# Optimization experiments

Hardware: AMD Instinct MI355X
Metric: run time of the kernel (lower is better)

The kernel has to match this reference:

```python
import jax, jax.numpy as jnp
import numpy as np

D_MODEL = 4096
NUM_EXPERTS = 64
TOP_K = 2


def setup_inputs() -> dict:
    key = jax.random.key(0)
    kx, kw, kb = jax.random.split(key, 3)
    x = jax.random.normal(kx, (4, 4096, D_MODEL), dtype=jnp.float32)
    # nn.Linear default init ~ U(-1/sqrt(fan_in), 1/sqrt(fan_in))
    bound = 1.0 / np.sqrt(D_MODEL)
    W = jax.random.uniform(kw, (D_MODEL, NUM_EXPERTS), minval=-bound, maxval=bound, dtype=jnp.float32)
    b = jax.random.uniform(kb, (NUM_EXPERTS,), minval=-bound, maxval=bound, dtype=jnp.float32)
    return {"x": x, "W": W, "b": b}


def reference(x, W, b):
    # gate: [B,S,D] @ [D,E] -> [B,S,E]
    logits = jnp.einsum('bsd,de->bse', x, W) + b
    probs = jax.nn.softmax(logits, axis=-1)
    topk_probs, topk_indices = jax.lax.top_k(probs, TOP_K)
    topk_probs = topk_probs / (jnp.sum(topk_probs, axis=-1, keepdims=True) + 1e-9)
    return probs, topk_probs, topk_indices
```

## Files before the change

### kernel.cpp

```cpp
#include <hip/hip_runtime.h>

#define D_MODEL 4096
#define NEXP    64
#define NTOK    16384
#define NKS     128

typedef _Float16 half8 __attribute__((ext_vector_type(8)));
typedef float    f32x4 __attribute__((ext_vector_type(4)));

__device__ __forceinline__ void split8(float4 a, float4 b, half8& hi, half8& lo) {
    auto h0 = __builtin_amdgcn_cvt_pkrtz(a.x, a.y);
    auto h1 = __builtin_amdgcn_cvt_pkrtz(a.z, a.w);
    auto h2 = __builtin_amdgcn_cvt_pkrtz(b.x, b.y);
    auto h3 = __builtin_amdgcn_cvt_pkrtz(b.z, b.w);
    hi[0] = static_cast<_Float16>(h0[0]); hi[1] = static_cast<_Float16>(h0[1]);
    hi[2] = static_cast<_Float16>(h1[0]); hi[3] = static_cast<_Float16>(h1[1]);
    hi[4] = static_cast<_Float16>(h2[0]); hi[5] = static_cast<_Float16>(h2[1]);
    hi[6] = static_cast<_Float16>(h3[0]); hi[7] = static_cast<_Float16>(h3[1]);
    float r0 = a.x - (float)h0[0], r1 = a.y - (float)h0[1];
    float r2 = a.z - (float)h1[0], r3 = a.w - (float)h1[1];
    float r4 = b.x - (float)h2[0], r5 = b.y - (float)h2[1];
    float r6 = b.z - (float)h3[0], r7 = b.w - (float)h3[1];
    auto l0 = __builtin_amdgcn_cvt_pkrtz(r0, r1);
    auto l1 = __builtin_amdgcn_cvt_pkrtz(r2, r3);
    auto l2 = __builtin_amdgcn_cvt_pkrtz(r4, r5);
    auto l3 = __builtin_amdgcn_cvt_pkrtz(r6, r7);
    lo[0] = static_cast<_Float16>(l0[0]); lo[1] = static_cast<_Float16>(l0[1]);
    lo[2] = static_cast<_Float16>(l1[0]); lo[3] = static_cast<_Float16>(l1[1]);
    lo[4] = static_cast<_Float16>(l2[0]); lo[5] = static_cast<_Float16>(l2[1]);
    lo[6] = static_cast<_Float16>(l3[0]); lo[7] = static_cast<_Float16>(l3[1]);
}

__device__ __forceinline__ void dma16(const float* g, float* l) {
    __builtin_amdgcn_global_load_lds(
        (const __attribute__((address_space(1))) unsigned int*)g,
        (__attribute__((address_space(3))) unsigned int*)l,
        16, 0, 0);
}

__global__ __launch_bounds__(256) void prep_w(const float* __restrict__ W,
                                              half8* __restrict__ ws) {
    const int gid  = blockIdx.x * 256 + threadIdx.x;
    const int lane = gid & 63;
    const int fp   = gid >> 6;
    const int t    = fp & 3;
    const int ks   = fp >> 2;
    const int e    = 16 * t + (lane & 15);
    const int k0   = ks * 32 + (lane >> 4) * 8;
    float4 a, b;
    a.x = W[(size_t)(k0 + 0) * NEXP + e];
    a.y = W[(size_t)(k0 + 1) * NEXP + e];
    a.z = W[(size_t)(k0 + 2) * NEXP + e];
    a.w = W[(size_t)(k0 + 3) * NEXP + e];
    b.x = W[(size_t)(k0 + 4) * NEXP + e];
    b.y = W[(size_t)(k0 + 5) * NEXP + e];
    b.z = W[(size_t)(k0 + 6) * NEXP + e];
    b.w = W[(size_t)(k0 + 7) * NEXP + e];
    half8 hi, lo;
    split8(a, b, hi, lo);
    ws[(size_t)(fp * 2 + 0) * 64 + lane] = hi;
    ws[(size_t)(fp * 2 + 1) * 64 + lane] = lo;
}

__global__ __launch_bounds__(256, 2) void router_mfma(
    const float* __restrict__ x, const int4* __restrict__ wf,
    const float* __restrict__ b, float* __restrict__ out)
{
    __shared__ float lds[4][4096];
    const int tid  = threadIdx.x;
    const int lane = tid & 63;
    const int wv   = tid >> 6;
    const int tok0 = blockIdx.x * 16;
    const int m    = lane & 15;
    const int q    = lane >> 4;
    const float* __restrict__ xrow =
        x + (size_t)(tok0 + m) * D_MODEL + wv * 1024 + q * 8;
    const int4* __restrict__ wq = wf + (size_t)wv * 32 * 512 + lane;
    float* __restrict__ xs = lds[wv];

    const int rot = (blockIdx.x ^ wv) & 7;

    f32x4 acc[4] = {};
    int4  wba[4][2], wbb[4][2];

    auto jof = [&](int bb) { return ((bb + rot) & 7) * 4; };

    auto stage = [&](int bb, int buf) {
        const int j0 = jof(bb);
        float* dst = xs + buf * 2048;
#pragma unroll
        for (int s = 0; s < 4; s++) {
            const float* src = xrow + (size_t)(j0 + s) * 32;
            dma16(src,     dst + (s * 2 + 0) * 256);
            dma16(src + 4, dst + (s * 2 + 1) * 256);
        }
    };
    auto ldw = [&](int4 (&w)[4][2], int j) {
        const int base = j * 512;
#pragma unroll
        for (int t = 0; t < 4; t++) {
            w[t][0] = wq[base + t * 128];
            w[t][1] = wq[base + t * 128 + 64];
        }
    };
    auto cmp = [&](int buf, int slot, int4 (&wb)[4][2]) {
        const float* px = xs + buf * 2048 + slot * 512 + lane * 4;
        float4 xa = *(const float4*)px;
        float4 xb = *(const float4*)(px + 256);
        half8 ahi, alo;
        split8(xa, xb, ahi, alo);
#pragma unroll
        for (int t = 0; t < 4; t++) {
            half8 bhi = __builtin_bit_cast(half8, wb[t][0]);
            half8 blo = __builtin_bit_cast(half8, wb[t][1]);
            acc[t] = __builtin_amdgcn_mfma_f32_16x16x32_f16(ahi, bhi, acc[t], 0, 0, 0);
            acc[t] = __builtin_amdgcn_mfma_f32_16x16x32_f16(ahi, blo, acc[t], 0, 0, 0);
            acc[t] = __builtin_amdgcn_mfma_f32_16x16x32_f16(alo, bhi, acc[t], 0, 0, 0);
        }
    };

    stage(0, 0);
    ldw(wba, jof(0));

#pragma unroll 1
    for (int bb = 0; bb < 8; bb++) {
        const int buf = bb & 1;
        if (bb < 7) {
            stage(bb + 1, buf ^ 1);
            asm volatile("s_waitcnt vmcnt(8)" ::: "memory");
        } else {
            asm volatile("s_waitcnt vmcnt(0)" ::: "memory");
        }
        __builtin_amdgcn_sched_barrier(0);
        const int j0 = jof(bb);
        const int jn = jof((bb + 1) & 7);
        ldw(wbb, j0 + 1); cmp(buf, 0, wba);
        ldw(wba, j0 + 2); cmp(buf, 1, wbb);
        ldw(wbb, j0 + 3); cmp(buf, 2, wba);
        ldw(wba, jn);     cmp(buf, 3, wbb);
    }

#pragma unroll
    for (int t = 0; t < 4; t++)
#pragma unroll
        for (int r = 0; r < 4; r++)
            xs[(q * 4 + r) * 68 + t * 16 + m] = acc[t][r];
    __syncthreads();

    const float bias = b[lane];
    float* __restrict__ probs_out = out;
    float* __restrict__ top_out   = out + (size_t)NTOK * NEXP;
    float* __restrict__ idx_out   = top_out + (size_t)NTOK * 2;

#pragma unroll 1
    for (int r2 = 0; r2 < 4; r2++) {
        const int row   = wv * 4 + r2;
        const int token = tok0 + row;
        float logit = lds[0][row * 68 + lane] + lds[1][row * 68 + lane]
                    + lds[2][row * 68 + lane] + lds[3][row * 68 + lane] + bias;

        float mx = logit;
#pragma unroll
        for (int off = 32; off; off >>= 1) mx = fmaxf(mx, __shfl_xor(mx, off, 64));
        float ex = expf(logit - mx);
        float s = ex;
#pragma unroll
        for (int off = 32; off; off >>= 1) s += __shfl_xor(s, off, 64);
        float p = ex / s;
        probs_out[(size_t)token * NEXP + lane] = p;

        float v = p; int idx = lane;
#pragma unroll
        for (int off = 32; off; off >>= 1) {
            float ov = __shfl_xor(v, off, 64);
            int   oi = __shfl_xor(idx, off, 64);
            if (ov > v || (ov == v && oi < idx)) { v = ov; idx = oi; }
        }
        const float v1 = v; const int i1 = idx;
        v = (lane == i1) ? -1.0f : p; idx = lane;
#pragma unroll
        for (int off = 32; off; off >>= 1) {
            float ov = __shfl_xor(v, off, 64);
            int   oi = __shfl_xor(idx, off, 64);
            if (ov > v || (ov == v && oi < idx)) { v = ov; idx = oi; }
        }
        const float v2 = v; const int i2 = idx;

        if (lane == 0) {
            const float dnm = v1 + v2 + 1e-9f;
            top_out[(size_t)token * 2 + 0] = v1 / dnm;
            top_out[(size_t)token * 2 + 1] = v2 / dnm;
            idx_out[(size_t)token * 2 + 0] = (float)i1;
            idx_out[(size_t)token * 2 + 1] = (float)i2;
        }
    }
}

#define BK  128
#define BKP (BK + 4)
__device__ __forceinline__ float rl(float v, int l) {
    return __int_as_float(__builtin_amdgcn_readlane(__float_as_int(v), l));
}
__global__ __launch_bounds__(128) void router_fallback(
    const float* __restrict__ x, const float* __restrict__ W,
    const float* __restrict__ b, float* __restrict__ out)
{
    __shared__ float wt[NEXP * BKP];
    const int tid  = threadIdx.x;
    const int lane = tid & 63;
    const int wv   = __builtin_amdgcn_readfirstlane(tid >> 6);
    const int tok0 = blockIdx.x * 16 + wv * 8;
    const float* __restrict__ xw = x + (size_t)tok0 * D_MODEL;

    float2 xcur[8], xnxt[8];
#pragma unroll
    for (int t = 0; t < 8; t++)
        xcur[t] = *(const float2*)(xw + (size_t)t * D_MODEL + 2 * lane);
    float accm[8];
#pragma unroll
    for (int t = 0; t < 8; t++) accm[t] = 0.f;

    for (int c = 0; c < D_MODEL / BK; c++) {
        const int k0 = c * BK;
        if (c + 1 < D_MODEL / BK) {
#pragma unroll
            for (int t = 0; t < 8; t++)
                xnxt[t] = *(const float2*)(xw + (size_t)t * D_MODEL + (k0 + BK) + 2 * lane);
        }
#pragma unroll
        for (int i = 0; i < 16; i++) {
            int n  = i * 128 + tid;
            int dd = n >> 4;
            int e0 = (n & 15) * 4;
            float4 v = *(const float4*)(W + (size_t)(k0 + dd) * NEXP + e0);
            wt[(e0 + 0) * BKP + dd] = v.x;
            wt[(e0 + 1) * BKP + dd] = v.y;
            wt[(e0 + 2) * BKP + dd] = v.z;
            wt[(e0 + 3) * BKP + dd] = v.w;
        }
        __syncthreads();
        float acc[8];
#pragma unroll
        for (int t = 0; t < 8; t++) acc[t] = 0.f;
        const float* wl = &wt[lane * BKP];
#pragma unroll 4
        for (int kk = 0; kk < BK; kk += 4) {
            float4 w4 = *(const float4*)(wl + kk);
            const int l0 = kk >> 1;
#pragma unroll
            for (int t = 0; t < 8; t++) {
                float a = acc[t];
                a = fmaf(rl(xcur[t].x, l0    ), w4.x, a);
                a = fmaf(rl(xcur[t].y, l0    ), w4.y, a);
                a = fmaf(rl(xcur[t].x, l0 + 1), w4.z, a);
                a = fmaf(rl(xcur[t].y, l0 + 1), w4.w, a);
                acc[t] = a;
            }
        }
#pragma unroll
        for (int t = 0; t < 8; t++) accm[t] += acc[t];
        __syncthreads();
#pragma unroll
        for (int t = 0; t < 8; t++) xcur[t] = xnxt[t];
    }

    const float bias = b[lane];
    float* __restrict__ probs_out = out;
    float* __restrict__ top_out   = out + (size_t)NTOK * NEXP;
    float* __restrict__ idx_out   = top_out + (size_t)NTOK * 2;
#pragma unroll 1
    for (int t = 0; t < 8; t++) {
        const int token = tok0 + t;
        float logit = accm[t] + bias;
        float mx = logit;
#pragma unroll
        for (int off = 32; off; off >>= 1) mx = fmaxf(mx, __shfl_xor(mx, off, 64));
        float ex = expf(logit - mx);
        float s = ex;
#pragma unroll
        for (int off = 32; off; off >>= 1) s += __shfl_xor(s, off, 64);
        float p = ex / s;
        probs_out[(size_t)token * NEXP + lane] = p;
        float v = p; int idx = lane;
#pragma unroll
        for (int off = 32; off; off >>= 1) {
            float ov = __shfl_xor(v, off, 64);
            int   oi = __shfl_xor(idx, off, 64);
            if (ov > v || (ov == v && oi < idx)) { v = ov; idx = oi; }
        }
        const float v1 = v; const int i1 = idx;
        v = (lane == i1) ? -1.0f : p; idx = lane;
#pragma unroll
        for (int off = 32; off; off >>= 1) {
            float ov = __shfl_xor(v, off, 64);
            int   oi = __shfl_xor(idx, off, 64);
            if (ov > v || (ov == v && oi < idx)) { v = ov; idx = oi; }
        }
        const float v2 = v; const int i2 = idx;
        if (lane == 0) {
            const float dnm = v1 + v2 + 1e-9f;
            top_out[(size_t)token * 2 + 0] = v1 / dnm;
            top_out[(size_t)token * 2 + 1] = v2 / dnm;
            idx_out[(size_t)token * 2 + 0] = (float)i1;
            idx_out[(size_t)token * 2 + 1] = (float)i2;
        }
    }
}

extern "C" void kernel_launch(void* const* d_in, const int* in_sizes, int n_in,
                              void* d_out, int out_size, void* d_ws, size_t ws_size,
                              hipStream_t stream) {
    const float* x = (const float*)d_in[0];
    const float* W = (const float*)d_in[1];
    const float* b = (const float*)d_in[2];
    float* out = (float*)d_out;

    const size_t need = (size_t)NKS * 4 * 2 * 64 * 16;
    if (ws_size >= need) {
        prep_w<<<128, 256, 0, stream>>>(W, (half8*)d_ws);
        router_mfma<<<NTOK / 16, 256, 0, stream>>>(x, (const int4*)d_ws, b, out);
    } else {
        router_fallback<<<NTOK / 16, 128, 0, stream>>>(x, W, b, out);
    }
}
```

Measured before the change: 392.0 us.

## Process 32 tokens per block to reuse loaded W fragments across two token tiles

Each block now handles 32 tokens instead of 16, with two accumulator sets, so every W fragment loaded into registers feeds two MFMA token tiles. This halves the W fetch traffic per token and the grid size. The x staging layout, rotation, and loop trip counts are restructured so each stage covers two k-chunks for both token tiles. In exchange it uses more accumulator registers and launches fewer blocks, which may hurt occupancy or latency hiding.

```diff
diff --git a/kernel.cpp b/kernel.cpp
--- a/kernel.cpp
+++ b/kernel.cpp
@@ -70,30 +70,35 @@
     const int tid  = threadIdx.x;
     const int lane = tid & 63;
     const int wv   = tid >> 6;
-    const int tok0 = blockIdx.x * 16;
+    const int tok0 = blockIdx.x * 32;
     const int m    = lane & 15;
     const int q    = lane >> 4;
-    const float* __restrict__ xrow =
-        x + (size_t)(tok0 + m) * D_MODEL + wv * 1024 + q * 8;
     const int4* __restrict__ wq = wf + (size_t)wv * 32 * 512 + lane;
     float* __restrict__ xs = lds[wv];
 
-    const int rot = (blockIdx.x ^ wv) & 7;
-
-    f32x4 acc[4] = {};
+    const int rot = (blockIdx.x ^ (wv << 2)) & 15;
+
+    const float* xsrc[4];
+#pragma unroll
+    for (int d = 0; d < 4; d++) {
+        const int tt = d >> 1, h = d & 1;
+        xsrc[d] = x + (size_t)(tok0 + tt * 16 + m) * D_MODEL
+                    + wv * 1024 + h * 16 + q * 4;
+    }
+
+    f32x4 acc[2][4] = {};
     int4  wba[4][2], wbb[4][2];
 
-    auto jof = [&](int bb) { return ((bb + rot) & 7) * 4; };
+    auto jof = [&](int bb) { return ((bb + rot) & 15) * 2; };
 
     auto stage = [&](int bb, int buf) {
         const int j0 = jof(bb);
         float* dst = xs + buf * 2048;
 #pragma unroll
-        for (int s = 0; s < 4; s++) {
-            const float* src = xrow + (size_t)(j0 + s) * 32;
-            dma16(src,     dst + (s * 2 + 0) * 256);
-            dma16(src + 4, dst + (s * 2 + 1) * 256);
-        }
+        for (int s = 0; s < 2; s++)
+#pragma unroll
+            for (int d = 0; d < 4; d++)
+                dma16(xsrc[d] + (size_t)(j0 + s) * 32, dst + s * 1024 + d * 256);
     };
     auto ldw = [&](int4 (&w)[4][2], int j) {
         const int base = j * 512;
@@ -103,19 +108,23 @@
             w[t][1] = wq[base + t * 128 + 64];
         }
     };
-    auto cmp = [&](int buf, int slot, int4 (&wb)[4][2]) {
-        const float* px = xs + buf * 2048 + slot * 512 + lane * 4;
-        float4 xa = *(const float4*)px;
-        float4 xb = *(const float4*)(px + 256);
-        half8 ahi, alo;
-        split8(xa, xb, ahi, alo);
-#pragma unroll
-        for (int t = 0; t < 4; t++) {
-            half8 bhi = __builtin_bit_cast(half8, wb[t][0]);
-            half8 blo = __builtin_bit_cast(half8, wb[t][1]);
-            acc[t] = __builtin_amdgcn_mfma_f32_16x16x32_f16(ahi, bhi, acc[t], 0, 0, 0);
-            acc[t] = __builtin_amdgcn_mfma_f32_16x16x32_f16(ahi, blo, acc[t], 0, 0, 0);
-            acc[t] = __builtin_amdgcn_mfma_f32_16x16x32_f16(alo, bhi, acc[t], 0, 0, 0);
+    auto cmp = [&](int buf, int s, int4 (&wb)[4][2]) {
+#pragma unroll
+        for (int tt = 0; tt < 2; tt++) {
+            const float* px = xs + buf * 2048 + s * 1024
+                            + (tt * 2 + (q >> 1)) * 256 + (q & 1) * 128 + m * 4;
+            float4 xa = *(const float4*)px;
+            float4 xb = *(const float4*)(px + 64);
+            half8 ahi, alo;
+            split8(xa, xb, ahi, alo);
+#pragma unroll
+            for (int t = 0; t < 4; t++) {
+                half8 bhi = __builtin_bit_cast(half8, wb[t][0]);
+                half8 blo = __builtin_bit_cast(half8, wb[t][1]);
+                acc[tt][t] = __builtin_amdgcn_mfma_f32_16x16x32_f16(ahi, bhi, acc[tt][t], 0, 0, 0);
+                acc[tt][t] = __builtin_amdgcn_mfma_f32_16x16x32_f16(ahi, blo, acc[tt][t], 0, 0, 0);
+                acc[tt][t] = __builtin_amdgcn_mfma_f32_16x16x32_f16(alo, bhi, acc[tt][t], 0, 0, 0);
+            }
         }
     };
 
@@ -123,28 +132,28 @@
     ldw(wba, jof(0));
 
 #pragma unroll 1
-    for (int bb = 0; bb < 8; bb++) {
+    for (int bb = 0; bb < 16; bb++) {
         const int buf = bb & 1;
-        if (bb < 7) {
+        if (bb < 15) {
             stage(bb + 1, buf ^ 1);
-            asm volatile("s_waitcnt vmcnt(8)" ::: "memory");
+            asm volatile("s_waitcnt vmcnt(16)" ::: "memory");
         } else {
             asm volatile("s_waitcnt vmcnt(0)" ::: "memory");
         }
         __builtin_amdgcn_sched_barrier(0);
         const int j0 = jof(bb);
-        const int jn = jof((bb + 1) & 7);
+        const int jn = jof((bb + 1) & 15);
         ldw(wbb, j0 + 1); cmp(buf, 0, wba);
-        ldw(wba, j0 + 2); cmp(buf, 1, wbb);
-        ldw(wbb, j0 + 3); cmp(buf, 2, wba);
-        ldw(wba, jn);     cmp(buf, 3, wbb);
-    }
-
-#pragma unroll
-    for (int t = 0; t < 4; t++)
-#pragma unroll
-        for (int r = 0; r < 4; r++)
-            xs[(q * 4 + r) * 68 + t * 16 + m] = acc[t][r];
+        ldw(wba, jn);     cmp(buf, 1, wbb);
+    }
+
+#pragma unroll
+    for (int tt = 0; tt < 2; tt++)
+#pragma unroll
+        for (int t = 0; t < 4; t++)
+#pragma unroll
+            for (int r = 0; r < 4; r++)
+                xs[(tt * 16 + q * 4 + r) * 68 + t * 16 + m] = acc[tt][t][r];
     __syncthreads();
 
     const float bias = b[lane];
@@ -153,8 +162,8 @@
     float* __restrict__ idx_out   = top_out + (size_t)NTOK * 2;
 
 #pragma unroll 1
-    for (int r2 = 0; r2 < 4; r2++) {
-        const int row   = wv * 4 + r2;
+    for (int r2 = 0; r2 < 8; r2++) {
+        const int row   = wv * 8 + r2;
         const int token = tok0 + row;
         float logit = lds[0][row * 68 + lane] + lds[1][row * 68 + lane]
                     + lds[2][row * 68 + lane] + lds[3][row * 68 + lane] + bias;
@@ -318,7 +327,7 @@
     const size_t need = (size_t)NKS * 4 * 2 * 64 * 16;
     if (ws_size >= need) {
         prep_w<<<128, 256, 0, stream>>>(W, (half8*)d_ws);
-        router_mfma<<<NTOK / 16, 256, 0, stream>>>(x, (const int4*)d_ws, b, out);
+        router_mfma<<<NTOK / 32, 256, 0, stream>>>(x, (const int4*)d_ws, b, out);
     } else {
         router_fallback<<<NTOK / 16, 128, 0, stream>>>(x, W, b, out);
     }
```

Result: no change. 385.3 us (-1.7%).
